# Kernel optimization log

Measured on AMD Instinct MI355X. Metric: run time of the kernel, lower is better.

## Reference

```python
import jax, jax.numpy as jnp
import numpy as np
from jax import lax

_SOBEL_X = jnp.array([[-1., 0., 1.], [-2., 0., 2.], [-1., 0., 1.]], dtype=jnp.float32)
_SOBEL_Y = jnp.array([[1., 2., 1.], [0., 0., 0.], [-1., -2., -1.]], dtype=jnp.float32)


def rgb2ycrcb(x):
    # x: [B,3,H,W] -> [B,3,H,W] (Y, Cr, Cb)
    R, G, B = x[:, 0], x[:, 1], x[:, 2]
    Y = 0.299 * R + 0.587 * G + 0.114 * B
    Cr = (R - Y) * 0.713 + 0.5
    Cb = (B - Y) * 0.564 + 0.5
    return jnp.stack([Y, Cr, Cb], axis=1)


def depthwise_sobel(x):
    # x: [B,3,H,W]; per-channel 3x3 cross-correlation with SAME padding (matches F.conv2d pad=1)
    C = x.shape[1]
    wx = jnp.broadcast_to(_SOBEL_X[None, None], (C, 1, 3, 3))
    wy = jnp.broadcast_to(_SOBEL_Y[None, None], (C, 1, 3, 3))
    dn = ('NCHW', 'OIHW', 'NCHW')
    gx = lax.conv_general_dilated(x, wx, (1, 1), 'SAME', feature_group_count=C, dimension_numbers=dn)
    gy = lax.conv_general_dilated(x, wy, (1, 1), 'SAME', feature_group_count=C, dimension_numbers=dn)
    return gx, gy


def adjust_gamma(img, gamma, gain=1.0):
    # torchvision float path: clamp(gain * img**gamma, 0, 1)
    return jnp.clip(gain * img ** gamma, 0.0, 1.0)


def adjust_contrast(img, factor):
    # torchvision: blend with per-image mean of grayscale, then clamp
    gray = 0.2989 * img[:, 0:1] + 0.587 * img[:, 1:2] + 0.114 * img[:, 2:3]
    mean = jnp.mean(gray, axis=(1, 2, 3), keepdims=True)
    return jnp.clip(factor * img + (1.0 - factor) * mean, 0.0, 1.0)


def l1(a, b):
    return jnp.mean(jnp.abs(a - b))


def fusion_loss(input_vis, input_ir, output, Mask):
    Fuse = output * Mask
    ycc_fuse = rgb2ycrcb(Fuse)
    Cr_F, Cb_F = ycc_fuse[:, 1:2], ycc_fuse[:, 2:3]

    R_vis = adjust_gamma(input_vis, 0.5, 1.0)
    ycc_vis = rgb2ycrcb(R_vis)
    Cr_V, Cb_V = ycc_vis[:, 1:2], ycc_vis[:, 2:3]

    R_ir = adjust_contrast(input_ir, 1.8)

    fgx, fgy = depthwise_sobel(Fuse)
    vgx, vgy = depthwise_sobel(R_vis)
    igx, igy = depthwise_sobel(R_ir)

    joint_gx = jnp.maximum(vgx, igx)
    joint_gy = jnp.maximum(vgy, igy)
    joint_int = jnp.maximum(R_vis, R_ir)

    con_loss = l1(Fuse, joint_int)
    grad_loss = 0.5 * l1(fgx, joint_gx) + 0.5 * l1(fgy, joint_gy)
    color_loss = l1(Cb_F, Cb_V) + l1(Cr_F, Cr_V)
    return 0.5 * con_loss + 0.2 * grad_loss + 1.0 * color_loss


def setup_inputs() -> dict:
    key = jax.random.key(0)
    k1, k2, k3, k4 = jax.random.split(key, 4)
    B, C, H, W = 16, 3, 512, 512
    return {
        'input_vis': jax.random.uniform(k1, (B, C, H, W), dtype=jnp.float32),
        'input_ir': jax.random.uniform(k2, (B, C, H, W), dtype=jnp.float32),
        'output': jax.random.uniform(k3, (B, C, H, W), dtype=jnp.float32),
        'Mask': jax.random.uniform(k4, (B, C, H, W), dtype=jnp.float32),
    }


def reference(input_vis, input_ir, output, Mask):
    return fusion_loss(input_vis, input_ir, output, Mask)
```

## Files before the change

### kernel.cpp

```cpp
#include <hip/hip_runtime.h>
#include <math.h>

#define Bn 16
#define Cn 3
#define Hn 512
#define Wn 512
#define HWn (Hn*Wn)
#define CHWn (Cn*HWn)
#define Rr 4

__device__ __forceinline__ float clamp01(float x) {
    return fminf(fmaxf(x, 0.0f), 1.0f);
}

__global__ __launch_bounds__(256) void gray_mean_kernel(
        const float* __restrict__ ir, float* __restrict__ ws)
{
    const int b = blockIdx.y;
    const int tid = threadIdx.x;
    const float* base = ir + (size_t)b * CHWn;

    float sr = 0.f, sg = 0.f, sb = 0.f;
#pragma unroll
    for (int k = 0; k < 8; ++k) {
        size_t px = (size_t)blockIdx.x * 8192 + (size_t)(k * 256 + tid) * 4;
        float4 r4 = *(const float4*)(base + px);
        float4 g4 = *(const float4*)(base + HWn + px);
        float4 b4 = *(const float4*)(base + 2 * HWn + px);
        sr += (r4.x + r4.y) + (r4.z + r4.w);
        sg += (g4.x + g4.y) + (g4.z + g4.w);
        sb += (b4.x + b4.y) + (b4.z + b4.w);
    }
    float s = 0.2989f * sr + 0.587f * sg + 0.114f * sb;

#pragma unroll
    for (int off = 32; off; off >>= 1) s += __shfl_down(s, off, 64);

    __shared__ float red[4];
    if ((tid & 63) == 0) red[tid >> 6] = s;
    __syncthreads();
    if (tid == 0) atomicAdd(&ws[b], (red[0] + red[1]) + (red[2] + red[3]));
}

template<bool GUARDED>
__device__ __forceinline__ void sobel_channels(
        const float* __restrict__ pv, const float* __restrict__ pi,
        const float* __restrict__ po, const float* __restrict__ pm,
        int y0, int x0, float moff,
        float& conA, float& gxA, float& gyA)
{
    const int ldl = (x0 > 0) ? 1 : 0;
    const int ldr = (x0 + 4 < Wn) ? 1 : 0;
    const float fl = (float)ldl, fr = (float)ldr;

#define DECL_SLOT(S)                                                          \
    float wf##S##_0, wf##S##_1, wf##S##_2, wf##S##_3, wf##S##_4, wf##S##_5;   \
    float wv##S##_0, wv##S##_1, wv##S##_2, wv##S##_3, wv##S##_4, wv##S##_5;   \
    float wi##S##_0, wi##S##_1, wi##S##_2, wi##S##_3, wi##S##_4, wi##S##_5;

#define LOAD_ROW(Y, S)                                                        \
    do {                                                                      \
        const int y_ = (Y);                                                   \
        if (!GUARDED || (unsigned)y_ < (unsigned)Hn) {                        \
            const size_t o = (size_t)y_ * Wn + x0;                            \
            float4 o4 = *(const float4*)(o_ + o);                             \
            float4 m4 = *(const float4*)(m_ + o);                             \
            float4 v4 = *(const float4*)(v_ + o);                             \
            float4 i4 = *(const float4*)(i_ + o);                             \
             \
            float oL = fl * o_[o - ldl];     float oR = fr * o_[o + 3 + ldr]; \
            float mL = fl * m_[o - ldl];     float mR = fr * m_[o + 3 + ldr]; \
            float vL = fl * v_[o - ldl];     float vR = fr * v_[o + 3 + ldr]; \
            float iL = fl * i_[o - ldl];     float iR = fr * i_[o + 3 + ldr]; \
            wf##S##_0 = oL * mL;     wf##S##_1 = o4.x * m4.x;                 \
            wf##S##_2 = o4.y * m4.y; wf##S##_3 = o4.z * m4.z;                 \
            wf##S##_4 = o4.w * m4.w; wf##S##_5 = oR * mR;                     \
            wv##S##_0 = clamp01(sqrtf(vL));   wv##S##_1 = clamp01(sqrtf(v4.x)); \
            wv##S##_2 = clamp01(sqrtf(v4.y)); wv##S##_3 = clamp01(sqrtf(v4.z)); \
            wv##S##_4 = clamp01(sqrtf(v4.w)); wv##S##_5 = clamp01(sqrtf(vR));   \
            wi##S##_0 = fl * clamp01(fmaf(1.8f, iL,   -moff));                \
            wi##S##_1 = clamp01(fmaf(1.8f, i4.x, -moff));                     \
            wi##S##_2 = clamp01(fmaf(1.8f, i4.y, -moff));                     \
            wi##S##_3 = clamp01(fmaf(1.8f, i4.z, -moff));                     \
            wi##S##_4 = clamp01(fmaf(1.8f, i4.w, -moff));                     \
            wi##S##_5 = fr * clamp01(fmaf(1.8f, iR,   -moff));                \
        } else {                                                              \
            wf##S##_0=0.f; wf##S##_1=0.f; wf##S##_2=0.f;                      \
            wf##S##_3=0.f; wf##S##_4=0.f; wf##S##_5=0.f;                      \
            wv##S##_0=0.f; wv##S##_1=0.f; wv##S##_2=0.f;                      \
            wv##S##_3=0.f; wv##S##_4=0.f; wv##S##_5=0.f;                      \
            wi##S##_0=0.f; wi##S##_1=0.f; wi##S##_2=0.f;                      \
            wi##S##_3=0.f; wi##S##_4=0.f; wi##S##_5=0.f;                      \
        }                                                                     \
    } while (0)

#define SOBEL_J(A, B, C, J0, J1, J2)                                          \
    do {                                                                      \
        float gxf = (wf##A##_##J2 - wf##A##_##J0) + 2.f * (wf##B##_##J2 - wf##B##_##J0) + (wf##C##_##J2 - wf##C##_##J0); \
        float gyf = (wf##A##_##J0 + 2.f * wf##A##_##J1 + wf##A##_##J2) - (wf##C##_##J0 + 2.f * wf##C##_##J1 + wf##C##_##J2); \
        float gxv = (wv##A##_##J2 - wv##A##_##J0) + 2.f * (wv##B##_##J2 - wv##B##_##J0) + (wv##C##_##J2 - wv##C##_##J0); \
        float gyv = (wv##A##_##J0 + 2.f * wv##A##_##J1 + wv##A##_##J2) - (wv##C##_##J0 + 2.f * wv##C##_##J1 + wv##C##_##J2); \
        float gxi = (wi##A##_##J2 - wi##A##_##J0) + 2.f * (wi##B##_##J2 - wi##B##_##J0) + (wi##C##_##J2 - wi##C##_##J0); \
        float gyi = (wi##A##_##J0 + 2.f * wi##A##_##J1 + wi##A##_##J2) - (wi##C##_##J0 + 2.f * wi##C##_##J1 + wi##C##_##J2); \
        gxA  += fabsf(gxf - fmaxf(gxv, gxi));                                 \
        gyA  += fabsf(gyf - fmaxf(gyv, gyi));                                 \
        conA += fabsf(wf##B##_##J1 - fmaxf(wv##B##_##J1, wi##B##_##J1));      \
    } while (0)

#define STEP(A, B, C)                                                         \
    SOBEL_J(A, B, C, 0, 1, 2); SOBEL_J(A, B, C, 1, 2, 3);                     \
    SOBEL_J(A, B, C, 2, 3, 4); SOBEL_J(A, B, C, 3, 4, 5)

#pragma unroll
    for (int c = 0; c < 3; ++c) {
        const float* v_ = pv + (size_t)c * HWn;
        const float* i_ = pi + (size_t)c * HWn;
        const float* o_ = po + (size_t)c * HWn;
        const float* m_ = pm + (size_t)c * HWn;

        DECL_SLOT(0) DECL_SLOT(1) DECL_SLOT(2)

        LOAD_ROW(y0 - 1, 0);
        LOAD_ROW(y0,     1);
        LOAD_ROW(y0 + 1, 2); STEP(0, 1, 2);
        LOAD_ROW(y0 + 2, 0); STEP(1, 2, 0);
        LOAD_ROW(y0 + 3, 1); STEP(2, 0, 1);
        LOAD_ROW(y0 + 4, 2); STEP(0, 1, 2);
    }
#undef STEP
#undef SOBEL_J
#undef LOAD_ROW
#undef DECL_SLOT
}

__global__ __launch_bounds__(256) void fusion_main_kernel(
        const float* __restrict__ vis, const float* __restrict__ ir,
        const float* __restrict__ outp, const float* __restrict__ mask,
        float* __restrict__ ws)
{
    const int tid = threadIdx.x;
    const int tx = tid & 127;
    const int sy = tid >> 7;
    const int b  = blockIdx.y;
    const int y0 = (blockIdx.x * 2 + sy) * Rr;
    const int x0 = tx * 4;

    const float mean_b = ws[b] * (1.0f / (float)HWn);
    const float moff = 0.8f * mean_b;

    const size_t bb = (size_t)b * CHWn;
    const float* pv = vis  + bb;
    const float* pi = ir   + bb;
    const float* po = outp + bb;
    const float* pm = mask + bb;

    float conA = 0.f, gxA = 0.f, gyA = 0.f;

    if (y0 > 0 && y0 + Rr < Hn) {
        sobel_channels<false>(pv, pi, po, pm, y0, x0, moff, conA, gxA, gyA);
    } else {
        sobel_channels<true >(pv, pi, po, pm, y0, x0, moff, conA, gxA, gyA);
    }

    float crA = 0.f, cbA = 0.f;
    {
        for (int y = y0; y < y0 + Rr; ++y) {
            size_t o = (size_t)y * Wn + x0;
            float4 oR = *(const float4*)(po + o);
            float4 oG = *(const float4*)(po + HWn + o);
            float4 oB = *(const float4*)(po + 2 * HWn + o);
            float4 mR = *(const float4*)(pm + o);
            float4 mG = *(const float4*)(pm + HWn + o);
            float4 mB = *(const float4*)(pm + 2 * HWn + o);
            float4 vR = *(const float4*)(pv + o);
            float4 vG = *(const float4*)(pv + HWn + o);
            float4 vB = *(const float4*)(pv + 2 * HWn + o);
#define COLOR_PX(FR, FG, FB, VR, VG, VB)                                      \
            do {                                                              \
                float fr = (FR), fg = (FG), fb = (FB);                        \
                float vr = (VR), vg = (VG), vb = (VB);                        \
                float fY = 0.299f * fr + 0.587f * fg + 0.114f * fb;           \
                float vY = 0.299f * vr + 0.587f * vg + 0.114f * vb;           \
                crA += fabsf((fr - fY) * 0.713f - (vr - vY) * 0.713f);        \
                cbA += fabsf((fb - fY) * 0.564f - (vb - vY) * 0.564f);        \
            } while (0)
            COLOR_PX(oR.x * mR.x, oG.x * mG.x, oB.x * mB.x,
                     clamp01(sqrtf(vR.x)), clamp01(sqrtf(vG.x)), clamp01(sqrtf(vB.x)));
            COLOR_PX(oR.y * mR.y, oG.y * mG.y, oB.y * mB.y,
                     clamp01(sqrtf(vR.y)), clamp01(sqrtf(vG.y)), clamp01(sqrtf(vB.y)));
            COLOR_PX(oR.z * mR.z, oG.z * mG.z, oB.z * mB.z,
                     clamp01(sqrtf(vR.z)), clamp01(sqrtf(vG.z)), clamp01(sqrtf(vB.z)));
            COLOR_PX(oR.w * mR.w, oG.w * mG.w, oB.w * mB.w,
                     clamp01(sqrtf(vR.w)), clamp01(sqrtf(vG.w)), clamp01(sqrtf(vB.w)));
#undef COLOR_PX
        }
    }

    auto wred = [](float x) {
#pragma unroll
        for (int off = 32; off; off >>= 1) x += __shfl_down(x, off, 64);
        return x;
    };
    conA = wred(conA); gxA = wred(gxA); gyA = wred(gyA);
    crA  = wred(crA);  cbA = wred(cbA);

    __shared__ float red[5][4];
    const int lane = tid & 63, w = tid >> 6;
    if (lane == 0) {
        red[0][w] = conA; red[1][w] = gxA; red[2][w] = gyA;
        red[3][w] = crA;  red[4][w] = cbA;
    }
    __syncthreads();
    if (tid < 5) {
        float s = (red[tid][0] + red[tid][1]) + (red[tid][2] + red[tid][3]);
        atomicAdd(&ws[16 + tid], s);
    }
}

__global__ void finalize_kernel(const float* __restrict__ ws, float* __restrict__ out)
{
    if (threadIdx.x == 0 && blockIdx.x == 0) {
        const float invN3 = 1.0f / (float)((size_t)Bn * Cn * HWn);
        const float invN1 = 1.0f / (float)((size_t)Bn * HWn);
        float con = ws[16] * invN3;
        float gx  = ws[17] * invN3;
        float gy  = ws[18] * invN3;
        float cr  = ws[19] * invN1;
        float cb  = ws[20] * invN1;
        out[0] = 0.5f * con + 0.2f * (0.5f * gx + 0.5f * gy) + (cb + cr);
    }
}

extern "C" void kernel_launch(void* const* d_in, const int* in_sizes, int n_in,
                              void* d_out, int out_size, void* d_ws, size_t ws_size,
                              hipStream_t stream)
{
    const float* vis = (const float*)d_in[0];
    const float* ir  = (const float*)d_in[1];
    const float* out = (const float*)d_in[2];
    const float* msk = (const float*)d_in[3];
    float* ws = (float*)d_ws;

    hipMemsetAsync(ws, 0, 32 * sizeof(float), stream);

    gray_mean_kernel<<<dim3(32, Bn), 256, 0, stream>>>(ir, ws);
    fusion_main_kernel<<<dim3(Hn / (2 * Rr), Bn), 256, 0, stream>>>(vis, ir, out, msk, ws);
    finalize_kernel<<<1, 64, 0, stream>>>(ws, (float*)d_out);
}
```

Before: 263.5 us.

## Stage tiles in LDS via global_load_lds and fuse color loss into sobel pass

```diff
diff --git a/kernel.cpp b/kernel.cpp
--- a/kernel.cpp
+++ b/kernel.cpp
@@ -11,6 +11,12 @@
 
 __device__ __forceinline__ float clamp01(float x) {
     return fminf(fmaxf(x, 0.0f), 1.0f);
+}
+
+__device__ __forceinline__ void gload_lds16(const float* g, float* l) {
+    __builtin_amdgcn_global_load_lds(
+        (const __attribute__((address_space(1))) void*)g,
+        (__attribute__((address_space(3))) void*)l, 16, 0, 0);
 }
 
 __global__ __launch_bounds__(256) void gray_mean_kernel(
@@ -42,36 +48,38 @@
     if (tid == 0) atomicAdd(&ws[b], (red[0] + red[1]) + (red[2] + red[3]));
 }
 
-template<bool GUARDED>
-__device__ __forceinline__ void sobel_channels(
-        const float* __restrict__ pv, const float* __restrict__ pi,
-        const float* __restrict__ po, const float* __restrict__ pm,
-        int y0, int x0, float moff,
-        float& conA, float& gxA, float& gyA)
-{
-    const int ldl = (x0 > 0) ? 1 : 0;
-    const int ldr = (x0 + 4 < Wn) ? 1 : 0;
-    const float fl = (float)ldl, fr = (float)ldr;
 
 #define DECL_SLOT(S)                                                          \
     float wf##S##_0, wf##S##_1, wf##S##_2, wf##S##_3, wf##S##_4, wf##S##_5;   \
     float wv##S##_0, wv##S##_1, wv##S##_2, wv##S##_3, wv##S##_4, wv##S##_5;   \
     float wi##S##_0, wi##S##_1, wi##S##_2, wi##S##_3, wi##S##_4, wi##S##_5;
 
-#define LOAD_ROW(Y, S)                                                        \
+#define DECL_COL(RO)                                                          \
+    float cfY_##RO##_1=0.f, cfY_##RO##_2=0.f, cfY_##RO##_3=0.f, cfY_##RO##_4=0.f; \
+    float cvY_##RO##_1=0.f, cvY_##RO##_2=0.f, cvY_##RO##_3=0.f, cvY_##RO##_4=0.f; \
+    float cfr_##RO##_1=0.f, cfr_##RO##_2=0.f, cfr_##RO##_3=0.f, cfr_##RO##_4=0.f; \
+    float cvr_##RO##_1=0.f, cvr_##RO##_2=0.f, cvr_##RO##_3=0.f, cvr_##RO##_4=0.f;
+
+#define LOAD_ROW_LDS(LL, S)                                                   \
     do {                                                                      \
-        const int y_ = (Y);                                                   \
-        if (!GUARDED || (unsigned)y_ < (unsigned)Hn) {                        \
-            const size_t o = (size_t)y_ * Wn + x0;                            \
-            float4 o4 = *(const float4*)(o_ + o);                             \
-            float4 m4 = *(const float4*)(m_ + o);                             \
-            float4 v4 = *(const float4*)(v_ + o);                             \
-            float4 i4 = *(const float4*)(i_ + o);                             \
-             \
-            float oL = fl * o_[o - ldl];     float oR = fr * o_[o + 3 + ldr]; \
-            float mL = fl * m_[o - ldl];     float mR = fr * m_[o + 3 + ldr]; \
-            float vL = fl * v_[o - ldl];     float vR = fr * v_[o + 3 + ldr]; \
-            float iL = fl * i_[o - ldl];     float iR = fr * i_[o + 3 + ldr]; \
+        const int rr_ = sy2 + (LL);                                           \
+        if (!GUARDED || (unsigned)(y0 - 1 + rr_) < (unsigned)Hn) {            \
+            const float4 o4 = *(const float4*)&lds[0][rr_][x0];               \
+            const float4 m4 = *(const float4*)&lds[1][rr_][x0];               \
+            const float4 v4 = *(const float4*)&lds[2][rr_][x0];               \
+            const float4 i4 = *(const float4*)&lds[3][rr_][x0];               \
+            const float4 oq = *(const float4*)&lds[0][rr_][x0 - 4*ldl];       \
+            const float4 mq = *(const float4*)&lds[1][rr_][x0 - 4*ldl];       \
+            const float4 vq = *(const float4*)&lds[2][rr_][x0 - 4*ldl];       \
+            const float4 iq = *(const float4*)&lds[3][rr_][x0 - 4*ldl];       \
+            const float4 oz = *(const float4*)&lds[0][rr_][x0 + 4*ldr];       \
+            const float4 mz = *(const float4*)&lds[1][rr_][x0 + 4*ldr];       \
+            const float4 vz = *(const float4*)&lds[2][rr_][x0 + 4*ldr];       \
+            const float4 iz = *(const float4*)&lds[3][rr_][x0 + 4*ldr];       \
+            const float oL = fl * oq.w, oR = fr * oz.x;                       \
+            const float mL = fl * mq.w, mR = fr * mz.x;                       \
+            const float vL = fl * vq.w, vR = fr * vz.x;                       \
+            const float iL = fl * iq.w, iR = fr * iz.x;                       \
             wf##S##_0 = oL * mL;     wf##S##_1 = o4.x * m4.x;                 \
             wf##S##_2 = o4.y * m4.y; wf##S##_3 = o4.z * m4.z;                 \
             wf##S##_4 = o4.w * m4.w; wf##S##_5 = oR * mR;                     \
@@ -94,7 +102,7 @@
         }                                                                     \
     } while (0)
 
-#define SOBEL_J(A, B, C, J0, J1, J2)                                          \
+#define SOBEL_J(A, B, C, J0, J1, J2, RO)                                      \
     do {                                                                      \
         float gxf = (wf##A##_##J2 - wf##A##_##J0) + 2.f * (wf##B##_##J2 - wf##B##_##J0) + (wf##C##_##J2 - wf##C##_##J0); \
         float gyf = (wf##A##_##J0 + 2.f * wf##A##_##J1 + wf##A##_##J2) - (wf##C##_##J0 + 2.f * wf##C##_##J1 + wf##C##_##J2); \
@@ -104,46 +112,77 @@
         float gyi = (wi##A##_##J0 + 2.f * wi##A##_##J1 + wi##A##_##J2) - (wi##C##_##J0 + 2.f * wi##C##_##J1 + wi##C##_##J2); \
         gxA  += fabsf(gxf - fmaxf(gxv, gxi));                                 \
         gyA  += fabsf(gyf - fmaxf(gyv, gyi));                                 \
-        conA += fabsf(wf##B##_##J1 - fmaxf(wv##B##_##J1, wi##B##_##J1));      \
+        float f1 = wf##B##_##J1, v1 = wv##B##_##J1;                           \
+        conA += fabsf(f1 - fmaxf(v1, wi##B##_##J1));                          \
+        cfY_##RO##_##J1 = fmaf(coefc, f1, cfY_##RO##_##J1);                   \
+        cvY_##RO##_##J1 = fmaf(coefc, v1, cvY_##RO##_##J1);                   \
+        if (c == 0) { cfr_##RO##_##J1 = f1; cvr_##RO##_##J1 = v1; }           \
+        if (c == 2) {                                                         \
+            crA += fabsf(0.713f * ((cfr_##RO##_##J1 - cfY_##RO##_##J1)        \
+                                 - (cvr_##RO##_##J1 - cvY_##RO##_##J1)));     \
+            cbA += fabsf(0.564f * ((f1 - cfY_##RO##_##J1)                     \
+                                 - (v1 - cvY_##RO##_##J1)));                  \
+        }                                                                     \
     } while (0)
 
-#define STEP(A, B, C)                                                         \
-    SOBEL_J(A, B, C, 0, 1, 2); SOBEL_J(A, B, C, 1, 2, 3);                     \
-    SOBEL_J(A, B, C, 2, 3, 4); SOBEL_J(A, B, C, 3, 4, 5)
-
-#pragma unroll
+#define STEP(A, B, C, RO)                                                     \
+    SOBEL_J(A, B, C, 0, 1, 2, RO); SOBEL_J(A, B, C, 1, 2, 3, RO);             \
+    SOBEL_J(A, B, C, 2, 3, 4, RO); SOBEL_J(A, B, C, 3, 4, 5, RO)
+
+template<bool GUARDED>
+__device__ __forceinline__ void fusion_body(
+        const float* __restrict__ pv, const float* __restrict__ pi,
+        const float* __restrict__ po, const float* __restrict__ pm,
+        int y0, int tid, float moff,
+        float& conA, float& gxA, float& gyA, float& crA, float& cbA,
+        float (&lds)[4][6][512])
+{
+    const int tx = tid & 127;
+    const int sy = tid >> 7;
+    const int sy2 = sy * 2;
+    const int x0 = tx * 4;
+    const int ldl = (x0 > 0) ? 1 : 0;
+    const int ldr = (x0 + 4 < Wn) ? 1 : 0;
+    const float fl = (float)ldl, fr = (float)ldr;
+    const int wv = tid >> 6;
+    const int lane = tid & 63;
+    const float* tb = (wv == 0) ? po : (wv == 1) ? pm : (wv == 2) ? pv : pi;
+
+    DECL_COL(0) DECL_COL(1)
+
+#pragma unroll 1
     for (int c = 0; c < 3; ++c) {
-        const float* v_ = pv + (size_t)c * HWn;
-        const float* i_ = pi + (size_t)c * HWn;
-        const float* o_ = po + (size_t)c * HWn;
-        const float* m_ = pm + (size_t)c * HWn;
+        const float coefc = (c == 0) ? 0.299f : (c == 1) ? 0.587f : 0.114f;
+        const float* tc = tb + (size_t)c * HWn;
+
+#pragma unroll
+        for (int k = 0; k < 12; ++k) {
+            const int r = k >> 1, h = k & 1;
+            int ys = y0 - 1 + r;
+            if (GUARDED) ys = ys < 0 ? 0 : (ys >= Hn ? Hn - 1 : ys);
+            gload_lds16(tc + (size_t)ys * Wn + h * 256 + lane * 4,
+                        &lds[wv][r][h * 256]);
+        }
+        __syncthreads();
 
         DECL_SLOT(0) DECL_SLOT(1) DECL_SLOT(2)
-
-        LOAD_ROW(y0 - 1, 0);
-        LOAD_ROW(y0,     1);
-        LOAD_ROW(y0 + 1, 2); STEP(0, 1, 2);
-        LOAD_ROW(y0 + 2, 0); STEP(1, 2, 0);
-        LOAD_ROW(y0 + 3, 1); STEP(2, 0, 1);
-        LOAD_ROW(y0 + 4, 2); STEP(0, 1, 2);
-    }
-#undef STEP
-#undef SOBEL_J
-#undef LOAD_ROW
-#undef DECL_SLOT
-}
-
-__global__ __launch_bounds__(256) void fusion_main_kernel(
+        LOAD_ROW_LDS(0, 0);
+        LOAD_ROW_LDS(1, 1);
+        LOAD_ROW_LDS(2, 2); STEP(0, 1, 2, 0);
+        LOAD_ROW_LDS(3, 0); STEP(1, 2, 0, 1);
+        __syncthreads();
+    }
+}
+
+__global__ __launch_bounds__(256, 3) void fusion_main_kernel(
         const float* __restrict__ vis, const float* __restrict__ ir,
         const float* __restrict__ outp, const float* __restrict__ mask,
         float* __restrict__ ws)
 {
+    __shared__ float lds[4][6][512];
     const int tid = threadIdx.x;
-    const int tx = tid & 127;
-    const int sy = tid >> 7;
-    const int b  = blockIdx.y;
-    const int y0 = (blockIdx.x * 2 + sy) * Rr;
-    const int x0 = tx * 4;
+    const int b   = blockIdx.y;
+    const int y0  = blockIdx.x * Rr;
 
     const float mean_b = ws[b] * (1.0f / (float)HWn);
     const float moff = 0.8f * mean_b;
@@ -154,47 +193,12 @@
     const float* po = outp + bb;
     const float* pm = mask + bb;
 
-    float conA = 0.f, gxA = 0.f, gyA = 0.f;
-
-    if (y0 > 0 && y0 + Rr < Hn) {
-        sobel_channels<false>(pv, pi, po, pm, y0, x0, moff, conA, gxA, gyA);
-    } else {
-        sobel_channels<true >(pv, pi, po, pm, y0, x0, moff, conA, gxA, gyA);
-    }
-
-    float crA = 0.f, cbA = 0.f;
-    {
-        for (int y = y0; y < y0 + Rr; ++y) {
-            size_t o = (size_t)y * Wn + x0;
-            float4 oR = *(const float4*)(po + o);
-            float4 oG = *(const float4*)(po + HWn + o);
-            float4 oB = *(const float4*)(po + 2 * HWn + o);
-            float4 mR = *(const float4*)(pm + o);
-            float4 mG = *(const float4*)(pm + HWn + o);
-            float4 mB = *(const float4*)(pm + 2 * HWn + o);
-            float4 vR = *(const float4*)(pv + o);
-            float4 vG = *(const float4*)(pv + HWn + o);
-            float4 vB = *(const float4*)(pv + 2 * HWn + o);
-#define COLOR_PX(FR, FG, FB, VR, VG, VB)                                      \
-            do {                                                              \
-                float fr = (FR), fg = (FG), fb = (FB);                        \
-                float vr = (VR), vg = (VG), vb = (VB);                        \
-                float fY = 0.299f * fr + 0.587f * fg + 0.114f * fb;           \
-                float vY = 0.299f * vr + 0.587f * vg + 0.114f * vb;           \
-                crA += fabsf((fr - fY) * 0.713f - (vr - vY) * 0.713f);        \
-                cbA += fabsf((fb - fY) * 0.564f - (vb - vY) * 0.564f);        \
-            } while (0)
-            COLOR_PX(oR.x * mR.x, oG.x * mG.x, oB.x * mB.x,
-                     clamp01(sqrtf(vR.x)), clamp01(sqrtf(vG.x)), clamp01(sqrtf(vB.x)));
-            COLOR_PX(oR.y * mR.y, oG.y * mG.y, oB.y * mB.y,
-                     clamp01(sqrtf(vR.y)), clamp01(sqrtf(vG.y)), clamp01(sqrtf(vB.y)));
-            COLOR_PX(oR.z * mR.z, oG.z * mG.z, oB.z * mB.z,
-                     clamp01(sqrtf(vR.z)), clamp01(sqrtf(vG.z)), clamp01(sqrtf(vB.z)));
-            COLOR_PX(oR.w * mR.w, oG.w * mG.w, oB.w * mB.w,
-                     clamp01(sqrtf(vR.w)), clamp01(sqrtf(vG.w)), clamp01(sqrtf(vB.w)));
-#undef COLOR_PX
-        }
-    }
+    float conA = 0.f, gxA = 0.f, gyA = 0.f, crA = 0.f, cbA = 0.f;
+
+    if (blockIdx.x == 0 || blockIdx.x == gridDim.x - 1)
+        fusion_body<true >(pv, pi, po, pm, y0, tid, moff, conA, gxA, gyA, crA, cbA, lds);
+    else
+        fusion_body<false>(pv, pi, po, pm, y0, tid, moff, conA, gxA, gyA, crA, cbA, lds);
 
     auto wred = [](float x) {
 #pragma unroll
@@ -204,18 +208,25 @@
     conA = wred(conA); gxA = wred(gxA); gyA = wred(gyA);
     crA  = wred(crA);  cbA = wred(cbA);
 
-    __shared__ float red[5][4];
+    float* red = &lds[0][0][0];
     const int lane = tid & 63, w = tid >> 6;
     if (lane == 0) {
-        red[0][w] = conA; red[1][w] = gxA; red[2][w] = gyA;
-        red[3][w] = crA;  red[4][w] = cbA;
+        red[0 * 4 + w] = conA; red[1 * 4 + w] = gxA; red[2 * 4 + w] = gyA;
+        red[3 * 4 + w] = crA;  red[4 * 4 + w] = cbA;
     }
     __syncthreads();
     if (tid < 5) {
-        float s = (red[tid][0] + red[tid][1]) + (red[tid][2] + red[tid][3]);
+        float s = (red[tid * 4 + 0] + red[tid * 4 + 1])
+                + (red[tid * 4 + 2] + red[tid * 4 + 3]);
         atomicAdd(&ws[16 + tid], s);
     }
 }
+
+#undef STEP
+#undef SOBEL_J
+#undef LOAD_ROW_LDS
+#undef DECL_COL
+#undef DECL_SLOT
 
 __global__ void finalize_kernel(const float* __restrict__ ws, float* __restrict__ out)
 {
@@ -244,6 +255,6 @@
     hipMemsetAsync(ws, 0, 32 * sizeof(float), stream);
 
     gray_mean_kernel<<<dim3(32, Bn), 256, 0, stream>>>(ir, ws);
-    fusion_main_kernel<<<dim3(Hn / (2 * Rr), Bn), 256, 0, stream>>>(vis, ir, out, msk, ws);
+    fusion_main_kernel<<<dim3(Hn / Rr, Bn), 256, 0, stream>>>(vis, ir, out, msk, ws);
     finalize_kernel<<<1, 64, 0, stream>>>(ws, (float*)d_out);
 }
```

Result: faster. 240.1 us (-8.9%).
